# Performance work log

Measured on AMD Instinct MI355X. Metric: run time of the kernel, lower is better.

## Reference

```python
import jax, jax.numpy as jnp
import numpy as np


def setup_inputs() -> dict:
    key = jax.random.key(0)
    k1, k2, k3 = jax.random.split(key, 3)
    B, N, C_IN, C_OUT = 8, 2048, 128, 64
    x = jax.random.normal(k1, (B, N, C_IN), dtype=jnp.float32)
    # Linear(c_in, c_out): weight [c_out, c_in], bias [c_out]
    W_adj = jax.random.normal(k2, (C_OUT, C_IN), dtype=jnp.float32) * (1.0 / np.sqrt(C_IN))
    b_adj = jax.random.normal(k3, (C_OUT,), dtype=jnp.float32) * 0.01
    return {"x": x, "W_adj": W_adj, "b_adj": b_adj}


def reference(x, W_adj, b_adj):
    # e_x = adj_projection(x): [B, N, C_out]
    e_x = jnp.einsum("bnc,oc->bno", x, W_adj) + b_adj
    # The original loop/concat builds all (i, j) pairs and takes per-pair
    # inner products; this is exactly the Gram matrix e_x @ e_x^T.
    lp = jax.nn.relu(jnp.tanh(jnp.einsum("bic,bjc->bij", e_x, e_x)))  # [B, N, N]
    num_neighbours = x.shape[1]
    node_feats = jnp.einsum("bij,bjc->bic", lp, e_x) / num_neighbours
    return node_feats, lp
```

## Files before the change

kernel.cpp:

```cpp
#include <hip/hip_runtime.h>
#include <hip/hip_bf16.h>


#define B_    8
#define N_    2048
#define D_    64
#define CIN_  128

typedef __bf16 bf16x8 __attribute__((ext_vector_type(8)));
typedef float f32x4  __attribute__((ext_vector_type(4)));

union FragU { uint4 u; bf16x8 f; };

static __device__ __forceinline__ bf16x8 ld_frag(const __hip_bfloat16* p) {
    FragU fu; fu.u = *reinterpret_cast<const uint4*>(p); return fu.f;
}

static __device__ __forceinline__ void split8(const float* p, bf16x8& hi, bf16x8& lo) {
    const float4 a = *reinterpret_cast<const float4*>(p);
    const float4 b = *reinterpret_cast<const float4*>(p + 4);
    const float v[8] = {a.x, a.y, a.z, a.w, b.x, b.y, b.z, b.w};
#pragma unroll
    for (int i = 0; i < 8; i++) {
        const __bf16 h = (__bf16)v[i];
        hi[i] = h;
        lo[i] = (__bf16)(v[i] - (float)h);
    }
}

static __device__ __forceinline__ bf16x8 cvt8(const float* p) {
    const float4 a = *reinterpret_cast<const float4*>(p);
    const float4 b = *reinterpret_cast<const float4*>(p + 4);
    bf16x8 r;
    r[0] = (__bf16)a.x; r[1] = (__bf16)a.y; r[2] = (__bf16)a.z; r[3] = (__bf16)a.w;
    r[4] = (__bf16)b.x; r[5] = (__bf16)b.y; r[6] = (__bf16)b.z; r[7] = (__bf16)b.w;
    return r;
}

__global__ __launch_bounds__(256) void ex_kernel(
    const float* __restrict__ x,
    const float* __restrict__ W,
    const float* __restrict__ bias,
    __hip_bfloat16* __restrict__ e_hi,
    __hip_bfloat16* __restrict__ e_lo,
    __hip_bfloat16* __restrict__ e_hiT)
{
    const int tid  = threadIdx.x;
    const int w    = tid >> 6;
    const int lane = tid & 63;
    const int quad = lane >> 4;
    const int l16  = lane & 15;
    const int m0   = blockIdx.x * 64 + w * 16;

    const float* xrow = x + (size_t)(m0 + l16) * CIN_;
    bf16x8 ah[4], al[4];
#pragma unroll
    for (int ks = 0; ks < 4; ks++)
        split8(xrow + ks * 32 + quad * 8, ah[ks], al[ks]);

    f32x4 acc[4];
#pragma unroll
    for (int nt = 0; nt < 4; nt++) acc[nt] = f32x4{0.f, 0.f, 0.f, 0.f};

#pragma unroll
    for (int ks = 0; ks < 4; ks++) {
#pragma unroll
        for (int nt = 0; nt < 4; nt++) {
            bf16x8 wh, wl;
            split8(W + (size_t)(nt * 16 + l16) * CIN_ + ks * 32 + quad * 8, wh, wl);
            acc[nt] = __builtin_amdgcn_mfma_f32_16x16x32_bf16(ah[ks], wh, acc[nt], 0, 0, 0);
            acc[nt] = __builtin_amdgcn_mfma_f32_16x16x32_bf16(ah[ks], wl, acc[nt], 0, 0, 0);
            acc[nt] = __builtin_amdgcn_mfma_f32_16x16x32_bf16(al[ks], wh, acc[nt], 0, 0, 0);
        }
    }

#pragma unroll
    for (int nt = 0; nt < 4; nt++) {
        const int chan = nt * 16 + l16;
        const float bv = bias[chan];
#pragma unroll
        for (int i = 0; i < 4; i++) {
            const int gr = m0 + quad * 4 + i;
            const float e = acc[nt][i] + bv;
            const __hip_bfloat16 hi = __float2bfloat16(e);
            const __hip_bfloat16 lo = __float2bfloat16(e - __bfloat162float(hi));
            e_hi[(size_t)gr * D_ + chan] = hi;
            e_lo[(size_t)gr * D_ + chan] = lo;
            const int bt = gr >> 11, ir = gr & (N_ - 1);
            e_hiT[((size_t)bt * D_ + chan) * N_ + ir] = hi;
        }
    }
}

#define LDE  72
#define LDT  136
#define LDF  132

__global__ __launch_bounds__(512) void fused_kernel(
    const __hip_bfloat16* __restrict__ e_hi,
    const __hip_bfloat16* __restrict__ e_lo,
    const __hip_bfloat16* __restrict__ e_hiT,
    float* __restrict__ out)
{
    __shared__ __align__(16) unsigned char smem[64 * LDF * 4 + 128 * LDE * 2 * 2 + 64 * LDT * 2];
    float*          sLpF  = (float*)smem;
    __hip_bfloat16* sEhi  = (__hip_bfloat16*)(smem + 64 * LDF * 4);
    __hip_bfloat16* sElo  = sEhi + 128 * LDE;
    __hip_bfloat16* sEhiT = sElo + 128 * LDE;

    const int b   = blockIdx.x;
    const int i0  = blockIdx.y * 64;
    const int tid = threadIdx.x;
    const int w = tid >> 6, lane = tid & 63, quad = lane >> 4, l16 = lane & 15;
    const int g = w >> 1, h = w & 1;
    const int m0 = i0 + g * 16;

    const __hip_bfloat16* eih = e_hi + (size_t)(b * N_ + m0 + l16) * D_;
    const __hip_bfloat16* eil = e_lo + (size_t)(b * N_ + m0 + l16) * D_;
    bf16x8 ahi[2], alo[2];
#pragma unroll
    for (int ks = 0; ks < 2; ks++) {
        ahi[ks] = ld_frag(eih + ks * 32 + quad * 8);
        alo[ks] = ld_frag(eil + ks * 32 + quad * 8);
    }

    f32x4 o[4];
#pragma unroll
    for (int nt = 0; nt < 4; nt++) o[nt] = f32x4{0.f, 0.f, 0.f, 0.f};

    float* lp_out = out + (size_t)B_ * N_ * D_;

    for (int jt = 0; jt < 16; jt++) {
        const int j0 = jt * 128;
        __syncthreads();

#pragma unroll
        for (int p = 0; p < 2; p++) {
            const int q = tid + p * 512;
            {
                const int r = q >> 3, c = (q & 7) * 8;
                *(uint4*)(sEhi + r * LDE + c) =
                    *(const uint4*)(e_hi + (size_t)(b * N_ + j0 + r) * D_ + c);
                *(uint4*)(sElo + r * LDE + c) =
                    *(const uint4*)(e_lo + (size_t)(b * N_ + j0 + r) * D_ + c);
            }
            {
                const int r = q >> 4, c = (q & 15) * 8;
                *(uint4*)(sEhiT + r * LDT + c) =
                    *(const uint4*)(e_hiT + (size_t)(b * D_ + r) * N_ + j0 + c);
            }
        }
        __syncthreads();

#pragma unroll
        for (int nt = 0; nt < 4; nt++) {
            const int n0 = h * 64 + nt * 16;
            f32x4 s = f32x4{0.f, 0.f, 0.f, 0.f};
#pragma unroll
            for (int ks = 0; ks < 2; ks++) {
                const int koff = ks * 32 + quad * 8;
                bf16x8 bhi = ld_frag(sEhi + (n0 + l16) * LDE + koff);
                bf16x8 blo = ld_frag(sElo + (n0 + l16) * LDE + koff);
                s = __builtin_amdgcn_mfma_f32_16x16x32_bf16(ahi[ks], bhi, s, 0, 0, 0);
                s = __builtin_amdgcn_mfma_f32_16x16x32_bf16(ahi[ks], blo, s, 0, 0, 0);
                s = __builtin_amdgcn_mfma_f32_16x16x32_bf16(alo[ks], bhi, s, 0, 0, 0);
            }
#pragma unroll
            for (int i = 0; i < 4; i++) {
                const float tc = fmaxf(s[i], 0.0f);
                const float z = __builtin_amdgcn_exp2f(tc * -2.8853900817779268f);
                const float v = (1.0f - z) * __builtin_amdgcn_rcpf(1.0f + z);
                const int row = g * 16 + quad * 4 + i;
                const int col = n0 + l16;
                sLpF[row * LDF + col] = v;
            }
        }
        __syncthreads();

#pragma unroll
        for (int ks = 0; ks < 2; ks++) {
            const int koff = h * 64 + ks * 32 + quad * 8;
            bf16x8 a = cvt8(sLpF + (g * 16 + l16) * LDF + koff);
#pragma unroll
            for (int nt = 0; nt < 4; nt++) {
                bf16x8 bfr = ld_frag(sEhiT + (nt * 16 + l16) * LDT + koff);
                o[nt] = __builtin_amdgcn_mfma_f32_16x16x32_bf16(a, bfr, o[nt], 0, 0, 0);
            }
        }

#pragma unroll
        for (int p = 0; p < 4; p++) {
            const int q = tid + p * 512;
            const int r = q >> 5, c = (q & 31) * 4;
            *(float4*)(lp_out + ((size_t)(b * N_ + i0 + r)) * N_ + j0 + c) =
                *(const float4*)(sLpF + r * LDF + c);
        }
    }

    __syncthreads();
    float* sO = (float*)smem;
#pragma unroll
    for (int nt = 0; nt < 4; nt++) {
#pragma unroll
        for (int i = 0; i < 4; i++) {
            const int row = quad * 4 + i;
            const int chan = nt * 16 + l16;
            sO[w * 1024 + row * 64 + chan] = o[nt][i];
        }
    }
    __syncthreads();
#pragma unroll
    for (int p = 0; p < 8; p++) {
        const int q = tid + p * 512;
        const int row = q >> 6, chan = q & 63;
        const int gg = row >> 4, rr = row & 15;
        const float v = sO[(2 * gg) * 1024 + rr * 64 + chan] +
                        sO[(2 * gg + 1) * 1024 + rr * 64 + chan];
        out[((size_t)(b * N_ + i0 + row)) * D_ + chan] = v * (1.0f / 2048.0f);
    }
}

extern "C" void kernel_launch(void* const* d_in, const int* in_sizes, int n_in,
                              void* d_out, int out_size, void* d_ws, size_t ws_size,
                              hipStream_t stream) {
    const float* x    = (const float*)d_in[0];
    const float* W    = (const float*)d_in[1];
    const float* bias = (const float*)d_in[2];
    float* out = (float*)d_out;

    __hip_bfloat16* e_hi  = (__hip_bfloat16*)d_ws;
    __hip_bfloat16* e_lo  = e_hi + (size_t)B_ * N_ * D_;
    __hip_bfloat16* e_hiT = e_lo + (size_t)B_ * N_ * D_;

    ex_kernel<<<dim3(256), dim3(256), 0, stream>>>(x, W, bias, e_hi, e_lo, e_hiT);
    fused_kernel<<<dim3(8, 32), dim3(512), 0, stream>>>(e_hi, e_lo, e_hiT, out);
}
```

Baseline: 179.4 us.

## Restructure fused Gram kernel with 32x32 MFMA, direct global loads, and staged e_x writes

The fused kernel now computes each 32x32 Gram tile with 32x32x16 MFMA, taking operands straight from global/L2 instead of staging them in shared memory. It writes lp directly to global from registers and keeps only a bf16 copy in LDS for the second GEMM, which drops most __syncthreads. Separately, W is pre-split into bf16 hi/lo by a small kernel, and ex_kernel stages its outputs in LDS so stores are coalesced, including the transpose. The risks are uncoalesced row-strided lp stores and reliance on a wave-local waitcnt instead of a barrier for the LDS hand-off.

```diff
diff --git a/kernel.cpp b/kernel.cpp
--- a/kernel.cpp
+++ b/kernel.cpp
@@ -9,6 +9,7 @@
 
 typedef __bf16 bf16x8 __attribute__((ext_vector_type(8)));
 typedef float f32x4  __attribute__((ext_vector_type(4)));
+typedef float f32x16 __attribute__((ext_vector_type(16)));
 
 union FragU { uint4 u; bf16x8 f; };
 
@@ -28,29 +29,46 @@
     }
 }
 
-static __device__ __forceinline__ bf16x8 cvt8(const float* p) {
-    const float4 a = *reinterpret_cast<const float4*>(p);
-    const float4 b = *reinterpret_cast<const float4*>(p + 4);
-    bf16x8 r;
-    r[0] = (__bf16)a.x; r[1] = (__bf16)a.y; r[2] = (__bf16)a.z; r[3] = (__bf16)a.w;
-    r[4] = (__bf16)b.x; r[5] = (__bf16)b.y; r[6] = (__bf16)b.z; r[7] = (__bf16)b.w;
-    return r;
+__global__ __launch_bounds__(256) void wsplit_kernel(
+    const float* __restrict__ W,
+    __hip_bfloat16* __restrict__ whi,
+    __hip_bfloat16* __restrict__ wlo)
+{
+    const int tid = threadIdx.x;
+#pragma unroll
+    for (int k = 0; k < 8; k++) {
+        const float4 v = reinterpret_cast<const float4*>(W)[tid * 8 + k];
+        const int idx = tid * 32 + k * 4;
+        const float vv[4] = {v.x, v.y, v.z, v.w};
+#pragma unroll
+        for (int j = 0; j < 4; j++) {
+            const __hip_bfloat16 h = __float2bfloat16(vv[j]);
+            whi[idx + j] = h;
+            wlo[idx + j] = __float2bfloat16(vv[j] - __bfloat162float(h));
+        }
+    }
 }
 
 __global__ __launch_bounds__(256) void ex_kernel(
     const float* __restrict__ x,
-    const float* __restrict__ W,
+    const __hip_bfloat16* __restrict__ whi,
+    const __hip_bfloat16* __restrict__ wlo,
     const float* __restrict__ bias,
     __hip_bfloat16* __restrict__ e_hi,
     __hip_bfloat16* __restrict__ e_lo,
     __hip_bfloat16* __restrict__ e_hiT)
 {
+    __shared__ __align__(16) __hip_bfloat16 sEh[64 * 72];
+    __shared__ __align__(16) __hip_bfloat16 sEl[64 * 72];
+    __shared__ __align__(16) __hip_bfloat16 sEt[64 * 72];
+
     const int tid  = threadIdx.x;
     const int w    = tid >> 6;
     const int lane = tid & 63;
     const int quad = lane >> 4;
     const int l16  = lane & 15;
-    const int m0   = blockIdx.x * 64 + w * 16;
+    const int gr0  = blockIdx.x * 64;
+    const int m0   = gr0 + w * 16;
 
     const float* xrow = x + (size_t)(m0 + l16) * CIN_;
     bf16x8 ah[4], al[4];
@@ -66,8 +84,8 @@
     for (int ks = 0; ks < 4; ks++) {
 #pragma unroll
         for (int nt = 0; nt < 4; nt++) {
-            bf16x8 wh, wl;
-            split8(W + (size_t)(nt * 16 + l16) * CIN_ + ks * 32 + quad * 8, wh, wl);
+            const bf16x8 wh = ld_frag(whi + (nt * 16 + l16) * CIN_ + ks * 32 + quad * 8);
+            const bf16x8 wl = ld_frag(wlo + (nt * 16 + l16) * CIN_ + ks * 32 + quad * 8);
             acc[nt] = __builtin_amdgcn_mfma_f32_16x16x32_bf16(ah[ks], wh, acc[nt], 0, 0, 0);
             acc[nt] = __builtin_amdgcn_mfma_f32_16x16x32_bf16(ah[ks], wl, acc[nt], 0, 0, 0);
             acc[nt] = __builtin_amdgcn_mfma_f32_16x16x32_bf16(al[ks], wh, acc[nt], 0, 0, 0);
@@ -80,21 +98,29 @@
         const float bv = bias[chan];
 #pragma unroll
         for (int i = 0; i < 4; i++) {
-            const int gr = m0 + quad * 4 + i;
+            const int rl = w * 16 + quad * 4 + i;
             const float e = acc[nt][i] + bv;
             const __hip_bfloat16 hi = __float2bfloat16(e);
             const __hip_bfloat16 lo = __float2bfloat16(e - __bfloat162float(hi));
-            e_hi[(size_t)gr * D_ + chan] = hi;
-            e_lo[(size_t)gr * D_ + chan] = lo;
-            const int bt = gr >> 11, ir = gr & (N_ - 1);
-            e_hiT[((size_t)bt * D_ + chan) * N_ + ir] = hi;
-        }
-    }
-}
-
-#define LDE  72
-#define LDT  136
-#define LDF  132
+            sEh[rl * 72 + chan] = hi;
+            sEl[rl * 72 + chan] = lo;
+            sEt[chan * 72 + rl] = hi;
+        }
+    }
+    __syncthreads();
+
+    const int bt = gr0 >> 11, ir0 = gr0 & (N_ - 1);
+#pragma unroll
+    for (int p = 0; p < 2; p++) {
+        const int q = tid + p * 256;
+        const int r = q >> 3, c = (q & 7) * 8;
+        *(uint4*)(e_hi + (size_t)(gr0 + r) * D_ + c)  = *(const uint4*)(sEh + r * 72 + c);
+        *(uint4*)(e_lo + (size_t)(gr0 + r) * D_ + c)  = *(const uint4*)(sEl + r * 72 + c);
+        *(uint4*)(e_hiT + ((size_t)bt * D_ + r) * N_ + ir0 + c) = *(const uint4*)(sEt + r * 72 + c);
+    }
+}
+
+#define LT 136
 
 __global__ __launch_bounds__(512) void fused_kernel(
     const __hip_bfloat16* __restrict__ e_hi,
@@ -102,121 +128,92 @@
     const __hip_bfloat16* __restrict__ e_hiT,
     float* __restrict__ out)
 {
-    __shared__ __align__(16) unsigned char smem[64 * LDF * 4 + 128 * LDE * 2 * 2 + 64 * LDT * 2];
-    float*          sLpF  = (float*)smem;
-    __hip_bfloat16* sEhi  = (__hip_bfloat16*)(smem + 64 * LDF * 4);
-    __hip_bfloat16* sElo  = sEhi + 128 * LDE;
-    __hip_bfloat16* sEhiT = sElo + 128 * LDE;
+    __shared__ __align__(16) __hip_bfloat16 sLp[64 * LT];
+    __shared__ __align__(16) float sO[8 * 32 * 64];
 
     const int b   = blockIdx.x;
     const int i0  = blockIdx.y * 64;
     const int tid = threadIdx.x;
-    const int w = tid >> 6, lane = tid & 63, quad = lane >> 4, l16 = lane & 15;
-    const int g = w >> 1, h = w & 1;
-    const int m0 = i0 + g * 16;
-
-    const __hip_bfloat16* eih = e_hi + (size_t)(b * N_ + m0 + l16) * D_;
-    const __hip_bfloat16* eil = e_lo + (size_t)(b * N_ + m0 + l16) * D_;
-    bf16x8 ahi[2], alo[2];
-#pragma unroll
-    for (int ks = 0; ks < 2; ks++) {
-        ahi[ks] = ld_frag(eih + ks * 32 + quad * 8);
-        alo[ks] = ld_frag(eil + ks * 32 + quad * 8);
-    }
-
-    f32x4 o[4];
-#pragma unroll
-    for (int nt = 0; nt < 4; nt++) o[nt] = f32x4{0.f, 0.f, 0.f, 0.f};
+    const int w = tid >> 6, lane = tid & 63;
+    const int l32 = lane & 31, half = lane >> 5;
+    const int quad = lane >> 4, l16 = lane & 15;
+    const int g2 = w >> 2, h2 = w & 3;
+
+    const __hip_bfloat16* eih = e_hi + (size_t)(b * N_ + i0 + g2 * 32 + l32) * D_;
+    const __hip_bfloat16* eil = e_lo + (size_t)(b * N_ + i0 + g2 * 32 + l32) * D_;
+    bf16x8 ahi[4], alo[4];
+#pragma unroll
+    for (int ks = 0; ks < 4; ks++) {
+        ahi[ks] = ld_frag(eih + ks * 16 + half * 8);
+        alo[ks] = ld_frag(eil + ks * 16 + half * 8);
+    }
+
+    f32x4 o[2][4];
+#pragma unroll
+    for (int mt = 0; mt < 2; mt++)
+#pragma unroll
+        for (int nt = 0; nt < 4; nt++) o[mt][nt] = f32x4{0.f, 0.f, 0.f, 0.f};
 
     float* lp_out = out + (size_t)B_ * N_ * D_;
 
     for (int jt = 0; jt < 16; jt++) {
         const int j0 = jt * 128;
-        __syncthreads();
-
-#pragma unroll
-        for (int p = 0; p < 2; p++) {
-            const int q = tid + p * 512;
-            {
-                const int r = q >> 3, c = (q & 7) * 8;
-                *(uint4*)(sEhi + r * LDE + c) =
-                    *(const uint4*)(e_hi + (size_t)(b * N_ + j0 + r) * D_ + c);
-                *(uint4*)(sElo + r * LDE + c) =
-                    *(const uint4*)(e_lo + (size_t)(b * N_ + j0 + r) * D_ + c);
+
+        const __hip_bfloat16* ejh = e_hi + (size_t)(b * N_ + j0 + h2 * 32 + l32) * D_;
+        const __hip_bfloat16* ejl = e_lo + (size_t)(b * N_ + j0 + h2 * 32 + l32) * D_;
+        f32x16 s = {};
+#pragma unroll
+        for (int ks = 0; ks < 4; ks++) {
+            const bf16x8 bh = ld_frag(ejh + ks * 16 + half * 8);
+            const bf16x8 bl = ld_frag(ejl + ks * 16 + half * 8);
+            s = __builtin_amdgcn_mfma_f32_32x32x16_bf16(ahi[ks], bh, s, 0, 0, 0);
+            s = __builtin_amdgcn_mfma_f32_32x32x16_bf16(ahi[ks], bl, s, 0, 0, 0);
+            s = __builtin_amdgcn_mfma_f32_32x32x16_bf16(alo[ks], bh, s, 0, 0, 0);
+        }
+
+#pragma unroll
+        for (int r = 0; r < 16; r++) {
+            const int rl = (r & 3) + 8 * (r >> 2) + 4 * half;
+            const float tc = fmaxf(s[r], 0.0f);
+            const float z = __builtin_amdgcn_exp2f(tc * -2.8853900817779268f);
+            const float v = (1.0f - z) * __builtin_amdgcn_rcpf(1.0f + z);
+            lp_out[(size_t)(b * N_ + i0 + g2 * 32 + rl) * N_ + j0 + h2 * 32 + l32] = v;
+            sLp[(g2 * 32 + rl) * LT + h2 * 32 + l32] = __float2bfloat16(v);
+        }
+
+        __builtin_amdgcn_s_waitcnt(0xc07f);
+
+#pragma unroll
+        for (int mt = 0; mt < 2; mt++) {
+            const bf16x8 a = ld_frag(sLp + (g2 * 32 + mt * 16 + l16) * LT + h2 * 32 + quad * 8);
+#pragma unroll
+            for (int nt = 0; nt < 4; nt++) {
+                const bf16x8 bfr = ld_frag(e_hiT + ((size_t)b * D_ + nt * 16 + l16) * N_
+                                           + j0 + h2 * 32 + quad * 8);
+                o[mt][nt] = __builtin_amdgcn_mfma_f32_16x16x32_bf16(a, bfr, o[mt][nt], 0, 0, 0);
             }
-            {
-                const int r = q >> 4, c = (q & 15) * 8;
-                *(uint4*)(sEhiT + r * LDT + c) =
-                    *(const uint4*)(e_hiT + (size_t)(b * D_ + r) * N_ + j0 + c);
-            }
-        }
-        __syncthreads();
-
-#pragma unroll
-        for (int nt = 0; nt < 4; nt++) {
-            const int n0 = h * 64 + nt * 16;
-            f32x4 s = f32x4{0.f, 0.f, 0.f, 0.f};
-#pragma unroll
-            for (int ks = 0; ks < 2; ks++) {
-                const int koff = ks * 32 + quad * 8;
-                bf16x8 bhi = ld_frag(sEhi + (n0 + l16) * LDE + koff);
-                bf16x8 blo = ld_frag(sElo + (n0 + l16) * LDE + koff);
-                s = __builtin_amdgcn_mfma_f32_16x16x32_bf16(ahi[ks], bhi, s, 0, 0, 0);
-                s = __builtin_amdgcn_mfma_f32_16x16x32_bf16(ahi[ks], blo, s, 0, 0, 0);
-                s = __builtin_amdgcn_mfma_f32_16x16x32_bf16(alo[ks], bhi, s, 0, 0, 0);
-            }
-#pragma unroll
-            for (int i = 0; i < 4; i++) {
-                const float tc = fmaxf(s[i], 0.0f);
-                const float z = __builtin_amdgcn_exp2f(tc * -2.8853900817779268f);
-                const float v = (1.0f - z) * __builtin_amdgcn_rcpf(1.0f + z);
-                const int row = g * 16 + quad * 4 + i;
-                const int col = n0 + l16;
-                sLpF[row * LDF + col] = v;
-            }
-        }
-        __syncthreads();
-
-#pragma unroll
-        for (int ks = 0; ks < 2; ks++) {
-            const int koff = h * 64 + ks * 32 + quad * 8;
-            bf16x8 a = cvt8(sLpF + (g * 16 + l16) * LDF + koff);
-#pragma unroll
-            for (int nt = 0; nt < 4; nt++) {
-                bf16x8 bfr = ld_frag(sEhiT + (nt * 16 + l16) * LDT + koff);
-                o[nt] = __builtin_amdgcn_mfma_f32_16x16x32_bf16(a, bfr, o[nt], 0, 0, 0);
-            }
-        }
-
-#pragma unroll
-        for (int p = 0; p < 4; p++) {
-            const int q = tid + p * 512;
-            const int r = q >> 5, c = (q & 31) * 4;
-            *(float4*)(lp_out + ((size_t)(b * N_ + i0 + r)) * N_ + j0 + c) =
-                *(const float4*)(sLpF + r * LDF + c);
         }
     }
 
     __syncthreads();
-    float* sO = (float*)smem;
-#pragma unroll
-    for (int nt = 0; nt < 4; nt++) {
-#pragma unroll
-        for (int i = 0; i < 4; i++) {
-            const int row = quad * 4 + i;
-            const int chan = nt * 16 + l16;
-            sO[w * 1024 + row * 64 + chan] = o[nt][i];
-        }
-    }
+#pragma unroll
+    for (int mt = 0; mt < 2; mt++)
+#pragma unroll
+        for (int nt = 0; nt < 4; nt++)
+#pragma unroll
+            for (int i = 0; i < 4; i++)
+                sO[w * 2048 + (mt * 16 + quad * 4 + i) * 64 + nt * 16 + l16] = o[mt][nt][i];
     __syncthreads();
 #pragma unroll
     for (int p = 0; p < 8; p++) {
         const int q = tid + p * 512;
         const int row = q >> 6, chan = q & 63;
-        const int gg = row >> 4, rr = row & 15;
-        const float v = sO[(2 * gg) * 1024 + rr * 64 + chan] +
-                        sO[(2 * gg + 1) * 1024 + rr * 64 + chan];
-        out[((size_t)(b * N_ + i0 + row)) * D_ + chan] = v * (1.0f / 2048.0f);
+        const int gg = row >> 5, rl = row & 31;
+        float v = 0.f;
+#pragma unroll
+        for (int hh = 0; hh < 4; hh++)
+            v += sO[(gg * 4 + hh) * 2048 + rl * 64 + chan];
+        out[(size_t)(b * N_ + i0 + row) * D_ + chan] = v * (1.0f / 2048.0f);
     }
 }
 
@@ -231,7 +228,10 @@
     __hip_bfloat16* e_hi  = (__hip_bfloat16*)d_ws;
     __hip_bfloat16* e_lo  = e_hi + (size_t)B_ * N_ * D_;
     __hip_bfloat16* e_hiT = e_lo + (size_t)B_ * N_ * D_;
-
-    ex_kernel<<<dim3(256), dim3(256), 0, stream>>>(x, W, bias, e_hi, e_lo, e_hiT);
+    __hip_bfloat16* whi   = e_hiT + (size_t)B_ * N_ * D_;
+    __hip_bfloat16* wlo   = whi + D_ * CIN_;
+
+    wsplit_kernel<<<dim3(1), dim3(256), 0, stream>>>(W, whi, wlo);
+    ex_kernel<<<dim3(256), dim3(256), 0, stream>>>(x, whi, wlo, bias, e_hi, e_lo, e_hiT);
     fused_kernel<<<dim3(8, 32), dim3(512), 0, stream>>>(e_hi, e_lo, e_hiT, out);
 }
```

Result: slower. 184.3 us (+2.7%).
